# Performance work log

Hardware: AMD Instinct MI355X
Metric: run time of the kernel (lower is better)

## Reference

```python
import jax, jax.numpy as jnp
import numpy as np

B, LMAX, NCOND, NHID = 256, 512, 300, 600

def setup_inputs() -> dict:
    key = jax.random.key(0)
    ks = jax.random.split(key, 7)
    x = jax.random.normal(ks[0], (B, NCOND), dtype=jnp.float32)
    context = jax.random.normal(ks[1], (B, LMAX, NCOND), dtype=jnp.float32)
    lengths = jax.random.randint(ks[2], (B,), 0, LMAX, dtype=jnp.int32)
    W1 = jax.random.normal(ks[3], (NCOND, NHID), dtype=jnp.float32) * (1.0 / np.sqrt(NCOND))
    b1 = jax.random.normal(ks[4], (NHID,), dtype=jnp.float32) * 0.02
    Wa = jax.random.normal(ks[5], (NHID, NCOND), dtype=jnp.float32) * (1.0 / np.sqrt(NHID))
    ba = jax.random.normal(ks[6], (NCOND,), dtype=jnp.float32) * 0.02
    return {"x": x, "context": context, "lengths": lengths, "W1": W1, "b1": b1, "Wa": Wa, "ba": ba}

def reference(x, context, lengths, W1, b1, Wa, ba):
    # lengths clamped to >=1 (a ragged context is always non-empty)
    lens = jnp.maximum(lengths, 1)
    # valid-position mask over padded context: [B, L, 1]
    valid = (jnp.arange(LMAX)[None, :] < lens[:, None])[..., None].astype(context.dtype)
    # per-token MLP: relu(ctx @ W1 + b1)  -> [B, L, nhid]
    h = jax.nn.relu(jnp.einsum('blc,ch->blh', context, W1) + b1)
    # masked mean over valid tokens (ragged mean-pool) -> [B, nhid]
    pooled = jnp.sum(h * valid, axis=1) / lens[:, None].astype(context.dtype)
    # sigmoid gate -> [B, ncond], applied to x embeddings
    gate = jax.nn.sigmoid(jnp.einsum('bh,hc->bc', pooled, Wa) + ba)
    return gate * x
```

## Files before the change

### kernel.cpp

```cpp
#include <hip/hip_runtime.h>
#include <math.h>

#define BB     256
#define LMAX   512
#define NCOND  300
#define NHID   600
#define NSEG   8
#define CHUNK  64
#define KPAD   320
#define KLDS   328
#define NCOLP  640
#define NKC    10

typedef short s16x8 __attribute__((ext_vector_type(8)));
typedef float f32x4 __attribute__((ext_vector_type(4)));

__device__ inline unsigned short f2bf(float f) {
    unsigned int x = __float_as_uint(f);
    x += 0x7fffu + ((x >> 16) & 1u);
    return (unsigned short)(x >> 16);
}

__global__ __launch_bounds__(256) void k0_w1t(const float* __restrict__ W1,
                                              unsigned short* __restrict__ w1t)
{
    const int t     = blockIdx.x * 256 + threadIdx.x;
    const int lane  = t & 63;
    const int g     = t >> 6;
    const int ntile = g / NKC;
    const int kc    = g - ntile * NKC;
    const int n     = ntile * 16 + (lane & 15);
    const int kbase = kc * 32 + (lane >> 4) * 8;
    union { unsigned short us[8]; s16x8 v8; } u;
#pragma unroll
    for (int j = 0; j < 8; ++j) {
        const int k = kbase + j;
        const float w = (n < NHID && k < NCOND) ? W1[(size_t)k * NHID + n] : 0.f;
        u.us[j] = f2bf(w);
    }
    *(s16x8*)(w1t + (size_t)t * 8) = u.v8;
}

__global__ __launch_bounds__(256, 3) void k1_mfma_pool(
    const float* __restrict__ ctx, const int* __restrict__ lengths,
    const unsigned short* __restrict__ w1t, const float* __restrict__ b1,
    float* __restrict__ partial)
{
    const int b  = blockIdx.x;
    const int s  = blockIdx.y;
    const int ch = blockIdx.z;

    int count = lengths[b]; if (count < 1) count = 1;
    const int l0 = s * CHUNK;
    if (l0 >= count) return;
    const int valid = min(count - l0, CHUNK);

    const int tid  = threadIdx.x;
    const int lane = tid & 63;
    const int wv   = tid >> 6;
    const int ln15 = lane & 15;
    const int kg   = lane >> 4;

    __shared__ __align__(16) unsigned short atile[CHUNK * KLDS];

#pragma unroll
    for (int p = 0; p < 10; ++p) {
        const int i  = p * 256 + tid;
        const int r  = i / 40;
        const int c8 = i - r * 40;
        union { unsigned short us[8]; s16x8 v8; } u;
        if (r < valid && c8 < 38) {
            const float* src = ctx + ((size_t)b * LMAX + l0 + r) * NCOND + c8 * 8;
            const float4 v0 = *(const float4*)src;
            float4 v1 = make_float4(0.f, 0.f, 0.f, 0.f);
            if (c8 < 37) v1 = *(const float4*)(src + 4);
            u.us[0] = f2bf(v0.x); u.us[1] = f2bf(v0.y);
            u.us[2] = f2bf(v0.z); u.us[3] = f2bf(v0.w);
            u.us[4] = f2bf(v1.x); u.us[5] = f2bf(v1.y);
            u.us[6] = f2bf(v1.z); u.us[7] = f2bf(v1.w);
        } else {
#pragma unroll
            for (int j = 0; j < 8; ++j) u.us[j] = 0;
        }
        *(s16x8*)(atile + r * KLDS + c8 * 8) = u.v8;
    }
    __syncthreads();

    const int ntile0 = ch * 20 + wv * 5;
    const unsigned short* bbase = w1t + ((size_t)ntile0 * NKC * 64 + lane) * 8;
    const unsigned short* arow  = atile + ln15 * KLDS + kg * 8;

    f32x4 acc[5][4];
#pragma unroll
    for (int nt = 0; nt < 5; ++nt)
#pragma unroll
        for (int mt = 0; mt < 4; ++mt) acc[nt][mt] = (f32x4){0.f, 0.f, 0.f, 0.f};

    s16x8 bf[2][5];
#pragma unroll
    for (int nt = 0; nt < 5; ++nt) bf[0][nt] = *(const s16x8*)(bbase + nt * 5120);

#pragma unroll
    for (int kc = 0; kc < NKC; ++kc) {
        const int cur = kc & 1, nxt = cur ^ 1;
        if (kc < NKC - 1) {
#pragma unroll
            for (int nt = 0; nt < 5; ++nt)
                bf[nxt][nt] = *(const s16x8*)(bbase + nt * 5120 + (kc + 1) * 512);
        }
        s16x8 af[4];
#pragma unroll
        for (int mt = 0; mt < 4; ++mt)
            af[mt] = *(const s16x8*)(arow + mt * 16 * KLDS + kc * 32);
#pragma unroll
        for (int nt = 0; nt < 5; ++nt)
#pragma unroll
            for (int mt = 0; mt < 4; ++mt)
                acc[nt][mt] = __builtin_amdgcn_mfma_f32_16x16x32_bf16(
                    af[mt], bf[cur][nt], acc[nt][mt], 0, 0, 0);
    }

#pragma unroll
    for (int nt = 0; nt < 5; ++nt) {
        const int colg = ch * 320 + wv * 80 + nt * 16 + ln15;
        const float b1c = (colg < NHID) ? b1[colg] : 0.f;
        float ssum = 0.f;
#pragma unroll
        for (int mt = 0; mt < 4; ++mt) {
            const int rbase = mt * 16 + kg * 4;
#pragma unroll
            for (int r = 0; r < 4; ++r) {
                const float h = fmaxf(acc[nt][mt][r] + b1c, 0.f);
                if (rbase + r < valid) ssum += h;
            }
        }
        ssum += __shfl_xor(ssum, 16, 64);
        ssum += __shfl_xor(ssum, 32, 64);
        if (kg == 0 && colg < NHID)
            partial[((size_t)s * BB + b) * NHID + colg] = ssum;
    }
}

__global__ __launch_bounds__(640) void k2_gate(
    const float* __restrict__ x, const int* __restrict__ lengths,
    const float* __restrict__ partial, const float* __restrict__ Wa,
    const float* __restrict__ ba, float* __restrict__ out)
{
    const int b0  = blockIdx.x * 2;
    const int tid = threadIdx.x;

    __shared__ float pl[2][NHID];

    if (tid < NHID) {
#pragma unroll
        for (int bb = 0; bb < 2; ++bb) {
            int count = lengths[b0 + bb]; if (count < 1) count = 1;
            const int nch = (count + CHUNK - 1) >> 6;
            float ssum = 0.f;
            for (int sp = 0; sp < nch; ++sp)
                ssum += partial[((size_t)sp * BB + (b0 + bb)) * NHID + tid];
            pl[bb][tid] = ssum / (float)count;
        }
    }
    __syncthreads();

    if (tid < 2 * NCOND) {
        const int bb = tid / NCOND;
        const int n  = tid - bb * NCOND;
        const int b  = b0 + bb;
        float a0 = ba[n], a1 = 0.f, a2 = 0.f, a3 = 0.f;
        const float4* p4 = (const float4*)pl[bb];
        for (int h4 = 0; h4 < 148; h4 += 4) {
            const float4 pv0 = p4[h4];
            const float4 pv1 = p4[h4 + 1];
            const float4 pv2 = p4[h4 + 2];
            const float4 pv3 = p4[h4 + 3];
            const int hb = h4 * 4;
            a0 = fmaf(pv0.x, Wa[(size_t)(hb +  0) * NCOND + n], a0);
            a0 = fmaf(pv0.y, Wa[(size_t)(hb +  1) * NCOND + n], a0);
            a0 = fmaf(pv0.z, Wa[(size_t)(hb +  2) * NCOND + n], a0);
            a0 = fmaf(pv0.w, Wa[(size_t)(hb +  3) * NCOND + n], a0);
            a1 = fmaf(pv1.x, Wa[(size_t)(hb +  4) * NCOND + n], a1);
            a1 = fmaf(pv1.y, Wa[(size_t)(hb +  5) * NCOND + n], a1);
            a1 = fmaf(pv1.z, Wa[(size_t)(hb +  6) * NCOND + n], a1);
            a1 = fmaf(pv1.w, Wa[(size_t)(hb +  7) * NCOND + n], a1);
            a2 = fmaf(pv2.x, Wa[(size_t)(hb +  8) * NCOND + n], a2);
            a2 = fmaf(pv2.y, Wa[(size_t)(hb +  9) * NCOND + n], a2);
            a2 = fmaf(pv2.z, Wa[(size_t)(hb + 10) * NCOND + n], a2);
            a2 = fmaf(pv2.w, Wa[(size_t)(hb + 11) * NCOND + n], a2);
            a3 = fmaf(pv3.x, Wa[(size_t)(hb + 12) * NCOND + n], a3);
            a3 = fmaf(pv3.y, Wa[(size_t)(hb + 13) * NCOND + n], a3);
            a3 = fmaf(pv3.z, Wa[(size_t)(hb + 14) * NCOND + n], a3);
            a3 = fmaf(pv3.w, Wa[(size_t)(hb + 15) * NCOND + n], a3);
        }
        {
            const float4 pv0 = p4[148];
            const float4 pv1 = p4[149];
            a0 = fmaf(pv0.x, Wa[(size_t)592 * NCOND + n], a0);
            a0 = fmaf(pv0.y, Wa[(size_t)593 * NCOND + n], a0);
            a0 = fmaf(pv0.z, Wa[(size_t)594 * NCOND + n], a0);
            a0 = fmaf(pv0.w, Wa[(size_t)595 * NCOND + n], a0);
            a1 = fmaf(pv1.x, Wa[(size_t)596 * NCOND + n], a1);
            a1 = fmaf(pv1.y, Wa[(size_t)597 * NCOND + n], a1);
            a1 = fmaf(pv1.z, Wa[(size_t)598 * NCOND + n], a1);
            a1 = fmaf(pv1.w, Wa[(size_t)599 * NCOND + n], a1);
        }
        const float acc  = (a0 + a1) + (a2 + a3);
        const float gate = 1.0f / (1.0f + expf(-acc));
        out[(size_t)b * NCOND + n] = gate * x[(size_t)b * NCOND + n];
    }
}

extern "C" void kernel_launch(void* const* d_in, const int* in_sizes, int n_in,
                              void* d_out, int out_size, void* d_ws, size_t ws_size,
                              hipStream_t stream)
{
    const float* x       = (const float*)d_in[0];
    const float* ctx     = (const float*)d_in[1];
    const int*   lengths = (const int*)  d_in[2];
    const float* W1      = (const float*)d_in[3];
    const float* b1      = (const float*)d_in[4];
    const float* Wa      = (const float*)d_in[5];
    const float* ba      = (const float*)d_in[6];
    float*       out     = (float*)d_out;

    unsigned short* w1t     = (unsigned short*)d_ws;
    float*          partial = (float*)((char*)d_ws + 409600);

    k0_w1t<<<100, 256, 0, stream>>>(W1, w1t);
    k1_mfma_pool<<<dim3(BB, NSEG, 2), 256, 0, stream>>>(ctx, lengths, w1t, b1, partial);
    k2_gate<<<BB / 2, 640, 0, stream>>>(x, lengths, partial, Wa, ba, out);
}
```

Baseline: 298.8 us.

## Double block to 512 threads, split M rows across wave pairs with LDS reduction

The MFMA pooling kernel now runs 8 waves per block instead of 4. Each pair of waves shares the same N tiles but handles half of the 64 token rows, which halves the accumulator registers per wave. The partial column sums of the two waves are combined through shared memory before being written out. The context tile load is remapped so each thread handles one row with strided columns, and the aim is more waves in flight to hide global load latency. The cost is an extra barrier, an LDS reduction, and each wave loading the same W1 fragments twice.

```diff
diff --git a/kernel.cpp b/kernel.cpp
--- a/kernel.cpp
+++ b/kernel.cpp
@@ -9,7 +9,6 @@
 #define CHUNK  64
 #define KPAD   320
 #define KLDS   328
-#define NCOLP  640
 #define NKC    10
 
 typedef short s16x8 __attribute__((ext_vector_type(8)));
@@ -41,7 +40,7 @@
     *(s16x8*)(w1t + (size_t)t * 8) = u.v8;
 }
 
-__global__ __launch_bounds__(256, 3) void k1_mfma_pool(
+__global__ __launch_bounds__(512, 4) void k1_mfma_pool(
     const float* __restrict__ ctx, const int* __restrict__ lengths,
     const unsigned short* __restrict__ w1t, const float* __restrict__ b1,
     float* __restrict__ partial)
@@ -63,38 +62,39 @@
 
     __shared__ __align__(16) unsigned short atile[CHUNK * KLDS];
 
-#pragma unroll
-    for (int p = 0; p < 10; ++p) {
-        const int i  = p * 256 + tid;
-        const int r  = i / 40;
-        const int c8 = i - r * 40;
-        union { unsigned short us[8]; s16x8 v8; } u;
-        if (r < valid && c8 < 38) {
-            const float* src = ctx + ((size_t)b * LMAX + l0 + r) * NCOND + c8 * 8;
-            const float4 v0 = *(const float4*)src;
+    {
+        const int r      = tid >> 3;
+        const int c8base = tid & 7;
+        const bool inrow = (r < valid);
+        const float* rowp = ctx + ((size_t)b * LMAX + l0 + r) * NCOND;
+#pragma unroll
+        for (int p = 0; p < 5; ++p) {
+            const int c8 = c8base + p * 8;
+            float4 v0 = make_float4(0.f, 0.f, 0.f, 0.f);
             float4 v1 = make_float4(0.f, 0.f, 0.f, 0.f);
-            if (c8 < 37) v1 = *(const float4*)(src + 4);
+            if (inrow && c8 <= 37) v0 = *(const float4*)(rowp + c8 * 8);
+            if (inrow && c8 <= 36) v1 = *(const float4*)(rowp + c8 * 8 + 4);
+            union { unsigned short us[8]; s16x8 v8; } u;
             u.us[0] = f2bf(v0.x); u.us[1] = f2bf(v0.y);
             u.us[2] = f2bf(v0.z); u.us[3] = f2bf(v0.w);
             u.us[4] = f2bf(v1.x); u.us[5] = f2bf(v1.y);
             u.us[6] = f2bf(v1.z); u.us[7] = f2bf(v1.w);
-        } else {
-#pragma unroll
-            for (int j = 0; j < 8; ++j) u.us[j] = 0;
-        }
-        *(s16x8*)(atile + r * KLDS + c8 * 8) = u.v8;
-    }
-    __syncthreads();
-
-    const int ntile0 = ch * 20 + wv * 5;
+            *(s16x8*)(atile + r * KLDS + c8 * 8) = u.v8;
+        }
+    }
+    __syncthreads();
+
+    const int ntg   = wv >> 1;
+    const int mrow0 = (wv & 1) * 32;
+    const int ntile0 = ch * 20 + ntg * 5;
     const unsigned short* bbase = w1t + ((size_t)ntile0 * NKC * 64 + lane) * 8;
-    const unsigned short* arow  = atile + ln15 * KLDS + kg * 8;
-
-    f32x4 acc[5][4];
+    const unsigned short* arow  = atile + (mrow0 + ln15) * KLDS + kg * 8;
+
+    f32x4 acc[5][2];
 #pragma unroll
     for (int nt = 0; nt < 5; ++nt)
 #pragma unroll
-        for (int mt = 0; mt < 4; ++mt) acc[nt][mt] = (f32x4){0.f, 0.f, 0.f, 0.f};
+        for (int mt = 0; mt < 2; ++mt) acc[nt][mt] = (f32x4){0.f, 0.f, 0.f, 0.f};
 
     s16x8 bf[2][5];
 #pragma unroll
@@ -108,26 +108,30 @@
             for (int nt = 0; nt < 5; ++nt)
                 bf[nxt][nt] = *(const s16x8*)(bbase + nt * 5120 + (kc + 1) * 512);
         }
-        s16x8 af[4];
-#pragma unroll
-        for (int mt = 0; mt < 4; ++mt)
+        s16x8 af[2];
+#pragma unroll
+        for (int mt = 0; mt < 2; ++mt)
             af[mt] = *(const s16x8*)(arow + mt * 16 * KLDS + kc * 32);
 #pragma unroll
         for (int nt = 0; nt < 5; ++nt)
 #pragma unroll
-            for (int mt = 0; mt < 4; ++mt)
+            for (int mt = 0; mt < 2; ++mt)
                 acc[nt][mt] = __builtin_amdgcn_mfma_f32_16x16x32_bf16(
                     af[mt], bf[cur][nt], acc[nt][mt], 0, 0, 0);
     }
 
+    __syncthreads();
+    float* psums = (float*)atile;
+
+    float wsum[5];
 #pragma unroll
     for (int nt = 0; nt < 5; ++nt) {
-        const int colg = ch * 320 + wv * 80 + nt * 16 + ln15;
+        const int colg = ch * 320 + ntg * 80 + nt * 16 + ln15;
         const float b1c = (colg < NHID) ? b1[colg] : 0.f;
         float ssum = 0.f;
 #pragma unroll
-        for (int mt = 0; mt < 4; ++mt) {
-            const int rbase = mt * 16 + kg * 4;
+        for (int mt = 0; mt < 2; ++mt) {
+            const int rbase = mrow0 + mt * 16 + kg * 4;
 #pragma unroll
             for (int r = 0; r < 4; ++r) {
                 const float h = fmaxf(acc[nt][mt][r] + b1c, 0.f);
@@ -136,8 +140,24 @@
         }
         ssum += __shfl_xor(ssum, 16, 64);
         ssum += __shfl_xor(ssum, 32, 64);
-        if (kg == 0 && colg < NHID)
-            partial[((size_t)s * BB + b) * NHID + colg] = ssum;
+        wsum[nt] = ssum;
+    }
+    if (kg == 0) {
+#pragma unroll
+        for (int nt = 0; nt < 5; ++nt)
+            psums[(wv * 5 + nt) * 16 + ln15] = wsum[nt];
+    }
+    __syncthreads();
+
+    if ((wv & 1) == 0 && kg == 0) {
+#pragma unroll
+        for (int nt = 0; nt < 5; ++nt) {
+            const float tot = psums[(wv * 5 + nt) * 16 + ln15]
+                            + psums[((wv + 1) * 5 + nt) * 16 + ln15];
+            const int colg = ch * 320 + ntg * 80 + nt * 16 + ln15;
+            if (colg < NHID)
+                partial[((size_t)s * BB + b) * NHID + colg] = tot;
+        }
     }
 }
 
@@ -228,6 +248,6 @@
     float*          partial = (float*)((char*)d_ws + 409600);
 
     k0_w1t<<<100, 256, 0, stream>>>(W1, w1t);
-    k1_mfma_pool<<<dim3(BB, NSEG, 2), 256, 0, stream>>>(ctx, lengths, w1t, b1, partial);
+    k1_mfma_pool<<<dim3(BB, NSEG, 2), 512, 0, stream>>>(ctx, lengths, w1t, b1, partial);
     k2_gate<<<BB / 2, 640, 0, stream>>>(x, lengths, partial, Wa, ba, out);
 }
```

Measured after the change: 307.0 us. 1.03x slower.
